# Kernel tuning notes

Measured on AMD Instinct MI355X. Metric: run time of the kernel, lower is better.

The kernel has to match this reference:

```python
import jax, jax.numpy as jnp
import numpy as np

N_NODES = 100000
N_EDGES = 800000
IN_DIM = 128
OUT_DIM = 128


def setup_inputs() -> dict:
    key = jax.random.key(0)
    k_h, k_w, k_src, k_dst = jax.random.split(key, 4)
    h = jax.random.normal(k_h, (N_NODES, IN_DIM), dtype=jnp.float32)
    # xavier_normal_ with relu gain ~ sqrt(2) * sqrt(2/(fan_in+fan_out))
    gain = np.sqrt(2.0)
    std = gain * np.sqrt(2.0 / (IN_DIM + OUT_DIM))
    W = jax.random.normal(k_w, (OUT_DIM, IN_DIM), dtype=jnp.float32) * std
    src = jax.random.randint(k_src, (N_EDGES,), 0, N_NODES, dtype=jnp.int64)
    dst = jax.random.randint(k_dst, (N_EDGES,), 0, N_NODES, dtype=jnp.int64)
    return {"h": h, "W": W, "src": src, "dst": dst}


def reference(h, W, src, dst):
    # fc + ReLU is applied per-edge to the gathered src feature, then summed
    # over incoming edges per dst node. Since fc acts on src features only,
    # project once per node ([N, in] @ [in, out]) then gather per edge.
    proj = jax.nn.relu(jnp.matmul(h, W.T))          # [N, out_dim]
    msgs = proj[src]                                 # [E, out_dim] (gather)
    out = jax.ops.segment_sum(msgs, dst, num_segments=N_NODES)  # [N, out_dim]
    return out
```

## Files before the change

### kernel.cpp

```cpp
#include <hip/hip_runtime.h>
#include <hip/hip_bf16.h>

#define IN_DIM 128
#define OUT_DIM 128
#define CAP 32

typedef __attribute__((ext_vector_type(8))) short short8;
typedef __attribute__((ext_vector_type(8))) unsigned short ushort8;
typedef __attribute__((ext_vector_type(4))) float floatx4;

__device__ __forceinline__ unsigned short f2bf(float x) {
    union { float f; unsigned int u; } a; a.f = x;
    unsigned int u = a.u;
    unsigned int r = (u + 0x7fffu + ((u >> 16) & 1u)) >> 16;
    return (unsigned short)r;
}
__device__ __forceinline__ ushort2 f2bf2(float x, float y) {
    __hip_bfloat162 h2 = __float22bfloat162_rn(make_float2(x, y));
    union { __hip_bfloat162 h; ushort2 u; } c; c.h = h2; return c.u;
}
__device__ __forceinline__ float bf_lo(unsigned int v) {
    union { unsigned int u; float f; } a; a.u = v << 16; return a.f;
}
__device__ __forceinline__ float bf_hi(unsigned int v) {
    union { unsigned int u; float f; } a; a.u = v & 0xffff0000u; return a.f;
}

__global__ __launch_bounds__(256) void bucket_kernel(const int* __restrict__ src,
                                                     const int* __restrict__ dst,
                                                     int* __restrict__ counts,
                                                     int* __restrict__ edges, int E) {
    int e = blockIdx.x * 256 + threadIdx.x;
    if (e < E) {
        int d = dst[e];
        int pos = atomicAdd(&counts[d], 1);
        if (pos < CAP) edges[d * CAP + pos] = src[e];
    }
}

#define APAD 136

__global__ __launch_bounds__(256) void proj_kernel(const float* __restrict__ h,
                                                   const float* __restrict__ W,
                                                   unsigned short* __restrict__ projb,
                                                   int M) {
    __shared__ unsigned short As[64][APAD];
    __shared__ unsigned short Bs[128][APAD];

    const int t = threadIdx.x;
    const int wave = t >> 6;
    const int lane = t & 63;
    const int block_m = blockIdx.x * 64;

#pragma unroll
    for (int p = 0; p < 8; p++) {
        int c = p * 256 + t;
        int row = c >> 5;
        int ch  = c & 31;
        int gm = block_m + row;
        float4 v = make_float4(0.f, 0.f, 0.f, 0.f);
        if (gm < M) v = *(const float4*)&h[(size_t)gm * IN_DIM + ch * 4];
        ushort2 lo = f2bf2(v.x, v.y), hi = f2bf2(v.z, v.w);
        ushort4 b; b.x = lo.x; b.y = lo.y; b.z = hi.x; b.w = hi.y;
        *(ushort4*)&As[row][ch * 4] = b;
    }
#pragma unroll
    for (int p = 0; p < 16; p++) {
        int c = p * 256 + t;
        int row = c >> 5;
        int ch  = c & 31;
        float4 v = *(const float4*)&W[(size_t)row * IN_DIM + ch * 4];
        ushort2 lo = f2bf2(v.x, v.y), hi = f2bf2(v.z, v.w);
        ushort4 b; b.x = lo.x; b.y = lo.y; b.z = hi.x; b.w = hi.y;
        *(ushort4*)&Bs[row][ch * 4] = b;
    }
    __syncthreads();

    const int mrow = wave * 16 + (lane & 15);
    const int kq   = (lane >> 4) * 8;
    floatx4 acc[8] = {};

#pragma unroll
    for (int ks = 0; ks < 4; ks++) {
        short8 a = *(const short8*)&As[mrow][ks * 32 + kq];
#pragma unroll
        for (int nt = 0; nt < 8; nt++) {
            short8 b = *(const short8*)&Bs[nt * 16 + (lane & 15)][ks * 32 + kq];
            acc[nt] = __builtin_amdgcn_mfma_f32_16x16x32_bf16(a, b, acc[nt], 0, 0, 0);
        }
    }

    __syncthreads();
    {
        const int rloc = wave * 16 + (lane >> 4) * 4;
        const int col  = lane & 15;
#pragma unroll
        for (int nt = 0; nt < 8; nt++)
#pragma unroll
            for (int i = 0; i < 4; i++)
                As[rloc + i][nt * 16 + col] = f2bf(fmaxf(acc[nt][i], 0.f));
    }
    __syncthreads();
#pragma unroll
    for (int q = 0; q < 4; q++) {
        int c = q * 256 + t;
        int row = c >> 4;
        int ch  = c & 15;
        int gm = block_m + row;
        if (gm < M) {
            ushort8 v = *(const ushort8*)&As[row][ch * 8];
            *(ushort8*)&projb[(size_t)gm * OUT_DIM + ch * 8] = v;
        }
    }
}

__global__ __launch_bounds__(256) void gather_kernel(const unsigned short* __restrict__ projb,
                                                     const int* __restrict__ edges,
                                                     const int* __restrict__ counts,
                                                     float* __restrict__ out, int M) {
    const int node = blockIdx.x * 4 + (threadIdx.x >> 6);
    const int lane = threadIdx.x & 63;
    if (node >= M) return;

    int cnt = counts[node];
    if (cnt > CAP) cnt = CAP;
    const int beg = node * CAP;
    const int slot = lane >> 3;
    const int half = lane & 7;

    float acc[16] = {};

    for (int p = 0; p * 8 < cnt; p++) {
        int i = p * 8 + slot;
        if (i < cnt) {
            int s = edges[beg + i];
            const unsigned short* r = &projb[(size_t)s * OUT_DIM + half * 16];
            uint4 a = *(const uint4*)r;
            uint4 b = *(const uint4*)(r + 8);
            acc[0]  += bf_lo(a.x); acc[1]  += bf_hi(a.x);
            acc[2]  += bf_lo(a.y); acc[3]  += bf_hi(a.y);
            acc[4]  += bf_lo(a.z); acc[5]  += bf_hi(a.z);
            acc[6]  += bf_lo(a.w); acc[7]  += bf_hi(a.w);
            acc[8]  += bf_lo(b.x); acc[9]  += bf_hi(b.x);
            acc[10] += bf_lo(b.y); acc[11] += bf_hi(b.y);
            acc[12] += bf_lo(b.z); acc[13] += bf_hi(b.z);
            acc[14] += bf_lo(b.w); acc[15] += bf_hi(b.w);
        }
    }

#pragma unroll
    for (int d = 8; d <= 32; d <<= 1)
#pragma unroll
        for (int j = 0; j < 16; j++)
            acc[j] += __shfl_xor(acc[j], d, 64);

    if (slot == 0) {
        float* o = &out[(size_t)node * OUT_DIM + half * 16];
        *(float4*)(o + 0)  = make_float4(acc[0], acc[1], acc[2], acc[3]);
        *(float4*)(o + 4)  = make_float4(acc[4], acc[5], acc[6], acc[7]);
        *(float4*)(o + 8)  = make_float4(acc[8], acc[9], acc[10], acc[11]);
        *(float4*)(o + 12) = make_float4(acc[12], acc[13], acc[14], acc[15]);
    }
}

extern "C" void kernel_launch(void* const* d_in, const int* in_sizes, int n_in,
                              void* d_out, int out_size, void* d_ws, size_t ws_size,
                              hipStream_t stream) {
    const float* h   = (const float*)d_in[0];
    const float* W   = (const float*)d_in[1];
    const int*   src = (const int*)d_in[2];
    const int*   dst = (const int*)d_in[3];
    float* out = (float*)d_out;

    const int M = in_sizes[0] / IN_DIM;
    const int E = in_sizes[2];

    char* ws = (char*)d_ws;
    unsigned short* projb = (unsigned short*)ws;
    size_t off = (size_t)M * OUT_DIM * sizeof(unsigned short);
    off = (off + 255) & ~(size_t)255;
    int* counts = (int*)(ws + off);  off += (size_t)M * sizeof(int);
    off = (off + 255) & ~(size_t)255;
    int* edges  = (int*)(ws + off);  off += (size_t)M * CAP * sizeof(int);

    hipMemsetAsync(counts, 0, (size_t)M * sizeof(int), stream);

    bucket_kernel<<<(E + 255) / 256, 256, 0, stream>>>(src, dst, counts, edges, E);

    proj_kernel<<<(M + 63) / 64, 256, 0, stream>>>(h, W, projb, M);

    gather_kernel<<<(M + 3) / 4, 256, 0, stream>>>(projb, edges, counts, out, M);
}
```

Measured before the change: 209.9 us.

## Pre-convert W to bf16, load A fragments directly, and give one node per 16-lane group

W is converted to bf16 once, in extra blocks of the bucket kernel, so each projection block copies bf16 W instead of reconverting fp32. The projection kernel now loads h straight from global memory into MFMA A-fragment registers, which drops the A tile from LDS and reuses the B buffer for the output staging. The gather kernel maps one node to 16 lanes, each owning 8 columns, with two edges per iteration and no cross-lane shuffle reduction. This trades lane-level parallelism per node for fewer shuffles and more independent loads.

```diff
diff --git a/kernel.cpp b/kernel.cpp
--- a/kernel.cpp
+++ b/kernel.cpp
@@ -25,12 +25,33 @@
 __device__ __forceinline__ float bf_hi(unsigned int v) {
     union { unsigned int u; float f; } a; a.u = v & 0xffff0000u; return a.f;
 }
-
-__global__ __launch_bounds__(256) void bucket_kernel(const int* __restrict__ src,
-                                                     const int* __restrict__ dst,
-                                                     int* __restrict__ counts,
-                                                     int* __restrict__ edges, int E) {
-    int e = blockIdx.x * 256 + threadIdx.x;
+__device__ __forceinline__ short8 pack8(float4 v0, float4 v1) {
+    ushort2 a0 = f2bf2(v0.x, v0.y), a1 = f2bf2(v0.z, v0.w);
+    ushort2 a2 = f2bf2(v1.x, v1.y), a3 = f2bf2(v1.z, v1.w);
+    short8 r;
+    r[0] = (short)a0.x; r[1] = (short)a0.y; r[2] = (short)a1.x; r[3] = (short)a1.y;
+    r[4] = (short)a2.x; r[5] = (short)a2.y; r[6] = (short)a3.x; r[7] = (short)a3.y;
+    return r;
+}
+
+__global__ __launch_bounds__(256) void wcvt_bucket_kernel(const float* __restrict__ W,
+                                                          unsigned short* __restrict__ Wb,
+                                                          const int* __restrict__ src,
+                                                          const int* __restrict__ dst,
+                                                          int* __restrict__ counts,
+                                                          int* __restrict__ edges,
+                                                          int E, int nWBlocks) {
+    if ((int)blockIdx.x < nWBlocks) {
+        int i = blockIdx.x * 256 + threadIdx.x;
+        if (i < (IN_DIM * OUT_DIM) / 4) {
+            float4 v = *(const float4*)&W[(size_t)i * 4];
+            ushort2 lo = f2bf2(v.x, v.y), hi = f2bf2(v.z, v.w);
+            ushort4 b; b.x = lo.x; b.y = lo.y; b.z = hi.x; b.w = hi.y;
+            *(ushort4*)&Wb[(size_t)i * 4] = b;
+        }
+        return;
+    }
+    int e = (blockIdx.x - nWBlocks) * 256 + threadIdx.x;
     if (e < E) {
         int d = dst[e];
         int pos = atomicAdd(&counts[d], 1);
@@ -38,79 +59,73 @@
     }
 }
 
-#define APAD 136
+#define BPAD 136
 
 __global__ __launch_bounds__(256) void proj_kernel(const float* __restrict__ h,
-                                                   const float* __restrict__ W,
+                                                   const unsigned short* __restrict__ Wb,
                                                    unsigned short* __restrict__ projb,
                                                    int M) {
-    __shared__ unsigned short As[64][APAD];
-    __shared__ unsigned short Bs[128][APAD];
+    __shared__ unsigned short Bs[128][BPAD];
 
     const int t = threadIdx.x;
     const int wave = t >> 6;
     const int lane = t & 63;
+    const int q = lane >> 4;
+    const int r = lane & 15;
     const int block_m = blockIdx.x * 64;
 
 #pragma unroll
     for (int p = 0; p < 8; p++) {
         int c = p * 256 + t;
-        int row = c >> 5;
-        int ch  = c & 31;
-        int gm = block_m + row;
-        float4 v = make_float4(0.f, 0.f, 0.f, 0.f);
-        if (gm < M) v = *(const float4*)&h[(size_t)gm * IN_DIM + ch * 4];
-        ushort2 lo = f2bf2(v.x, v.y), hi = f2bf2(v.z, v.w);
-        ushort4 b; b.x = lo.x; b.y = lo.y; b.z = hi.x; b.w = hi.y;
-        *(ushort4*)&As[row][ch * 4] = b;
-    }
-#pragma unroll
-    for (int p = 0; p < 16; p++) {
+        int row = c >> 4;
+        int ch  = c & 15;
+        *(ushort8*)&Bs[row][ch * 8] = *(const ushort8*)&Wb[(size_t)row * IN_DIM + ch * 8];
+    }
+
+    const int grow = block_m + wave * 16 + r;
+    const bool ok = grow < M;
+    short8 afr[4];
+    {
+        const float* hp = &h[(size_t)grow * IN_DIM + q * 8];
+        float4 z = make_float4(0.f, 0.f, 0.f, 0.f);
+#pragma unroll
+        for (int ks = 0; ks < 4; ks++) {
+            float4 v0 = ok ? *(const float4*)(hp + ks * 32) : z;
+            float4 v1 = ok ? *(const float4*)(hp + ks * 32 + 4) : z;
+            afr[ks] = pack8(v0, v1);
+        }
+    }
+    __syncthreads();
+
+    floatx4 acc[8] = {};
+#pragma unroll
+    for (int ks = 0; ks < 4; ks++) {
+#pragma unroll
+        for (int nt = 0; nt < 8; nt++) {
+            short8 b = *(const short8*)&Bs[nt * 16 + r][ks * 32 + q * 8];
+            acc[nt] = __builtin_amdgcn_mfma_f32_16x16x32_bf16(afr[ks], b, acc[nt], 0, 0, 0);
+        }
+    }
+    __syncthreads();
+
+    {
+        const int rloc = wave * 16 + q * 4;
+#pragma unroll
+        for (int nt = 0; nt < 8; nt++)
+#pragma unroll
+            for (int i = 0; i < 4; i++)
+                Bs[rloc + i][nt * 16 + r] = f2bf(fmaxf(acc[nt][i], 0.f));
+    }
+    __syncthreads();
+
+#pragma unroll
+    for (int p = 0; p < 4; p++) {
         int c = p * 256 + t;
-        int row = c >> 5;
-        int ch  = c & 31;
-        float4 v = *(const float4*)&W[(size_t)row * IN_DIM + ch * 4];
-        ushort2 lo = f2bf2(v.x, v.y), hi = f2bf2(v.z, v.w);
-        ushort4 b; b.x = lo.x; b.y = lo.y; b.z = hi.x; b.w = hi.y;
-        *(ushort4*)&Bs[row][ch * 4] = b;
-    }
-    __syncthreads();
-
-    const int mrow = wave * 16 + (lane & 15);
-    const int kq   = (lane >> 4) * 8;
-    floatx4 acc[8] = {};
-
-#pragma unroll
-    for (int ks = 0; ks < 4; ks++) {
-        short8 a = *(const short8*)&As[mrow][ks * 32 + kq];
-#pragma unroll
-        for (int nt = 0; nt < 8; nt++) {
-            short8 b = *(const short8*)&Bs[nt * 16 + (lane & 15)][ks * 32 + kq];
-            acc[nt] = __builtin_amdgcn_mfma_f32_16x16x32_bf16(a, b, acc[nt], 0, 0, 0);
-        }
-    }
-
-    __syncthreads();
-    {
-        const int rloc = wave * 16 + (lane >> 4) * 4;
-        const int col  = lane & 15;
-#pragma unroll
-        for (int nt = 0; nt < 8; nt++)
-#pragma unroll
-            for (int i = 0; i < 4; i++)
-                As[rloc + i][nt * 16 + col] = f2bf(fmaxf(acc[nt][i], 0.f));
-    }
-    __syncthreads();
-#pragma unroll
-    for (int q = 0; q < 4; q++) {
-        int c = q * 256 + t;
         int row = c >> 4;
         int ch  = c & 15;
         int gm = block_m + row;
-        if (gm < M) {
-            ushort8 v = *(const ushort8*)&As[row][ch * 8];
-            *(ushort8*)&projb[(size_t)gm * OUT_DIM + ch * 8] = v;
-        }
+        if (gm < M)
+            *(ushort8*)&projb[(size_t)gm * OUT_DIM + ch * 8] = *(const ushort8*)&Bs[row][ch * 8];
     }
 }
 
@@ -118,49 +133,42 @@
                                                      const int* __restrict__ edges,
                                                      const int* __restrict__ counts,
                                                      float* __restrict__ out, int M) {
-    const int node = blockIdx.x * 4 + (threadIdx.x >> 6);
-    const int lane = threadIdx.x & 63;
+    const int t = threadIdx.x;
+    const int wave = t >> 6;
+    const int lane = t & 63;
+    const int sub = lane >> 4;
+    const int li  = lane & 15;
+    const int node = blockIdx.x * 16 + wave * 4 + sub;
     if (node >= M) return;
 
     int cnt = counts[node];
     if (cnt > CAP) cnt = CAP;
     const int beg = node * CAP;
-    const int slot = lane >> 3;
-    const int half = lane & 7;
-
-    float acc[16] = {};
-
-    for (int p = 0; p * 8 < cnt; p++) {
-        int i = p * 8 + slot;
-        if (i < cnt) {
-            int s = edges[beg + i];
-            const unsigned short* r = &projb[(size_t)s * OUT_DIM + half * 16];
-            uint4 a = *(const uint4*)r;
-            uint4 b = *(const uint4*)(r + 8);
-            acc[0]  += bf_lo(a.x); acc[1]  += bf_hi(a.x);
-            acc[2]  += bf_lo(a.y); acc[3]  += bf_hi(a.y);
-            acc[4]  += bf_lo(a.z); acc[5]  += bf_hi(a.z);
-            acc[6]  += bf_lo(a.w); acc[7]  += bf_hi(a.w);
-            acc[8]  += bf_lo(b.x); acc[9]  += bf_hi(b.x);
-            acc[10] += bf_lo(b.y); acc[11] += bf_hi(b.y);
-            acc[12] += bf_lo(b.z); acc[13] += bf_hi(b.z);
-            acc[14] += bf_lo(b.w); acc[15] += bf_hi(b.w);
-        }
-    }
-
-#pragma unroll
-    for (int d = 8; d <= 32; d <<= 1)
-#pragma unroll
-        for (int j = 0; j < 16; j++)
-            acc[j] += __shfl_xor(acc[j], d, 64);
-
-    if (slot == 0) {
-        float* o = &out[(size_t)node * OUT_DIM + half * 16];
-        *(float4*)(o + 0)  = make_float4(acc[0], acc[1], acc[2], acc[3]);
-        *(float4*)(o + 4)  = make_float4(acc[4], acc[5], acc[6], acc[7]);
-        *(float4*)(o + 8)  = make_float4(acc[8], acc[9], acc[10], acc[11]);
-        *(float4*)(o + 12) = make_float4(acc[12], acc[13], acc[14], acc[15]);
-    }
+
+    float acc[8] = {};
+    int p = 0;
+    for (; p + 1 < cnt; p += 2) {
+        int s0 = edges[beg + p];
+        int s1 = edges[beg + p + 1];
+        uint4 a = *(const uint4*)&projb[(size_t)s0 * OUT_DIM + li * 8];
+        uint4 b = *(const uint4*)&projb[(size_t)s1 * OUT_DIM + li * 8];
+        acc[0] += bf_lo(a.x) + bf_lo(b.x); acc[1] += bf_hi(a.x) + bf_hi(b.x);
+        acc[2] += bf_lo(a.y) + bf_lo(b.y); acc[3] += bf_hi(a.y) + bf_hi(b.y);
+        acc[4] += bf_lo(a.z) + bf_lo(b.z); acc[5] += bf_hi(a.z) + bf_hi(b.z);
+        acc[6] += bf_lo(a.w) + bf_lo(b.w); acc[7] += bf_hi(a.w) + bf_hi(b.w);
+    }
+    if (p < cnt) {
+        int s0 = edges[beg + p];
+        uint4 a = *(const uint4*)&projb[(size_t)s0 * OUT_DIM + li * 8];
+        acc[0] += bf_lo(a.x); acc[1] += bf_hi(a.x);
+        acc[2] += bf_lo(a.y); acc[3] += bf_hi(a.y);
+        acc[4] += bf_lo(a.z); acc[5] += bf_hi(a.z);
+        acc[6] += bf_lo(a.w); acc[7] += bf_hi(a.w);
+    }
+
+    float* o = &out[(size_t)node * OUT_DIM + li * 8];
+    *(float4*)(o + 0) = make_float4(acc[0], acc[1], acc[2], acc[3]);
+    *(float4*)(o + 4) = make_float4(acc[4], acc[5], acc[6], acc[7]);
 }
 
 extern "C" void kernel_launch(void* const* d_in, const int* in_sizes, int n_in,
@@ -179,15 +187,21 @@
     unsigned short* projb = (unsigned short*)ws;
     size_t off = (size_t)M * OUT_DIM * sizeof(unsigned short);
     off = (off + 255) & ~(size_t)255;
+    unsigned short* Wb = (unsigned short*)(ws + off);
+    off += (size_t)IN_DIM * OUT_DIM * sizeof(unsigned short);
+    off = (off + 255) & ~(size_t)255;
     int* counts = (int*)(ws + off);  off += (size_t)M * sizeof(int);
     off = (off + 255) & ~(size_t)255;
     int* edges  = (int*)(ws + off);  off += (size_t)M * CAP * sizeof(int);
 
+    const int nW      = (IN_DIM * OUT_DIM / 4 + 255) / 256;
+    const int nBucket = (E + 255) / 256;
+
     hipMemsetAsync(counts, 0, (size_t)M * sizeof(int), stream);
 
-    bucket_kernel<<<(E + 255) / 256, 256, 0, stream>>>(src, dst, counts, edges, E);
-
-    proj_kernel<<<(M + 63) / 64, 256, 0, stream>>>(h, W, projb, M);
-
-    gather_kernel<<<(M + 3) / 4, 256, 0, stream>>>(projb, edges, counts, out, M);
-}
+    wcvt_bucket_kernel<<<nW + nBucket, 256, 0, stream>>>(W, Wb, src, dst, counts, edges, E, nW);
+
+    proj_kernel<<<(M + 63) / 64, 256, 0, stream>>>(h, Wb, projb, M);
+
+    gather_kernel<<<(M + 15) / 16, 256, 0, stream>>>(projb, edges, counts, out, M);
+}
```

New measurement: 218.2 us. 4.0% more time.
